# Performance work log

Measured on AMD Instinct MI355X. Metric: run time of the kernel, lower is better.

## Reference

```python
import jax, jax.numpy as jnp
import numpy as np

B, L, HID, NH = 8, 512, 768, 12
D = HID // NH
T_HOP, T_EDGE = 32, 64


def setup_inputs() -> dict:
    key = jax.random.key(0)
    ks = jax.random.split(key, 18)
    f = lambda k, s, sc=1.0: jax.random.normal(k, s, dtype=jnp.float32) * sc
    return {
        "x": f(ks[0], (B, L, HID)),
        "query_hop_emb": f(ks[1], (T_HOP, HID), 0.05),
        "query_edge_emb": f(ks[2], (T_EDGE, HID), 0.05),
        "key_hop_emb": f(ks[3], (T_HOP, HID), 0.05),
        "key_edge_emb": f(ks[4], (T_EDGE, HID), 0.05),
        "value_hop_emb": f(ks[5], (T_HOP, HID), 0.05),
        "value_edge_emb": f(ks[6], (T_EDGE, HID), 0.05),
        "hop": jax.random.randint(ks[7], (B, L, L), 0, T_HOP, dtype=jnp.int32),
        "edge_matrix": jax.random.randint(ks[8], (B, L, L), 0, T_EDGE, dtype=jnp.int32),
        "Wq": f(ks[9], (HID, HID), 0.02), "bq": f(ks[10], (HID,), 0.02),
        "Wk": f(ks[11], (HID, HID), 0.02), "bk": f(ks[12], (HID,), 0.02),
        "Wv": f(ks[13], (HID, HID), 0.02), "bv": f(ks[14], (HID,), 0.02),
        "Wo": f(ks[15], (HID, HID), 0.02), "bo": f(ks[16], (HID,), 0.02),
    }


def reference(x, query_hop_emb, query_edge_emb, key_hop_emb, key_edge_emb,
              value_hop_emb, value_edge_emb, hop, edge_matrix,
              Wq, bq, Wk, bk, Wv, bv, Wo, bo):
    b, l, _ = x.shape
    scale = 1.0 / np.sqrt(D).astype(np.float32)
    heads = lambda t: t.reshape(b, l, NH, D).transpose(0, 2, 1, 3)  # [B,H,L,D]
    emb = lambda t: t.reshape(-1, NH, D)                             # [T,H,D]

    q = heads(x @ Wq + bq)
    k = heads(x @ Wk + bk)
    v = heads(x @ Wv + bv)

    hop_idx = jnp.broadcast_to(hop[:, None], (b, NH, l, l))
    edge_idx = jnp.broadcast_to(edge_matrix[:, None], (b, NH, l, l))

    def bias(t, e, idx):
        # project onto type embeddings then gather per (i,j) type: [B,H,L,L]
        proj = jnp.einsum('bhld,thd->bhlt', t, emb(e))
        return jnp.take_along_axis(proj, idx, axis=3)

    scores = jnp.einsum('bhld,bhmd->bhlm', q, k)
    scores = scores + bias(q, query_hop_emb, hop_idx) + bias(q, query_edge_emb, edge_idx)
    scores = scores + bias(k, key_hop_emb, hop_idx) + bias(k, key_edge_emb, edge_idx)
    att = jax.nn.softmax(scores * scale, axis=3)

    def scatter_by_type(a, idx, T):
        # re-aggregate attention weights per hop/edge type: [B,H,L,T]
        bi = jnp.arange(b)[:, None, None, None]
        hi = jnp.arange(NH)[None, :, None, None]
        li = jnp.arange(l)[None, None, :, None]
        return jnp.zeros((b, NH, l, T), a.dtype).at[bi, hi, li, idx].add(a)

    out = jnp.einsum('bhlm,bhmd->bhld', att, v)
    out = out + jnp.einsum('bhlt,thd->bhld', scatter_by_type(att, hop_idx, T_HOP), emb(value_hop_emb))
    out = out + jnp.einsum('bhlt,thd->bhld', scatter_by_type(att, edge_idx, T_EDGE), emb(value_edge_emb))

    out = out.transpose(0, 2, 1, 3).reshape(b, l, NH * D)
    return out @ Wo + bo
```

## Files before the change

kernel.cpp:

```cpp
#include <hip/hip_runtime.h>
#include <stdint.h>

#define B_   8
#define L_   512
#define HID_ 768
#define NH_  12
#define D_   64
#define BH_  96
#define TT_  96

typedef __attribute__((ext_vector_type(8))) short short8;
typedef __attribute__((ext_vector_type(4))) float fv4;

#define MFMA16(a, b, c) __builtin_amdgcn_mfma_f32_16x16x32_bf16((a), (b), (c), 0, 0, 0)

__device__ __forceinline__ float bf2f(uint16_t h) {
  union { uint32_t u; float f; } c; c.u = ((uint32_t)h) << 16; return c.f;
}
__device__ __forceinline__ uint16_t f2bf(float x) {
  union { float f; uint32_t u; } c; c.f = x;
  uint32_t r = (c.u + 0x7FFFu + ((c.u >> 16) & 1u)) >> 16;
  return (uint16_t)r;
}
__device__ __forceinline__ float clampf(float v, float lim) {
  return fminf(fmaxf(v, -lim), lim);
}

__device__ __forceinline__ void gld_lds16(const uint16_t* g, uint16_t* lds) {
  __builtin_amdgcn_global_load_lds(
      (const __attribute__((address_space(1))) uint32_t*)(uintptr_t)g,
      (__attribute__((address_space(3))) uint32_t*)(uintptr_t)lds, 16, 0, 0);
}

__device__ __forceinline__ int detect_fp32(const void* xraw) {
  const uint16_t* r = (const uint16_t*)xraw;
  int cnt = 0;
#pragma unroll
  for (int j = 0; j < 16; j++) {
    uint16_t u = r[2 * j];
    int e = (u >> 7) & 0xFF;
    if (u != 0 && e >= 100 && e <= 140) cnt++;
  }
  return cnt < 10;
}

#define SEG_X    0
#define SEG_QH   3145728
#define SEG_QE   3170304
#define SEG_KH   3219456
#define SEG_KE   3244032
#define SEG_VH   3293184
#define SEG_VE   3317760
#define SEG_BQ   3366912
#define SEG_BK   3367680
#define SEG_BV   3368448
#define SEG_BO   3369216
#define SEG_END  3369984
#define SEG_VET  3369984
#define SEG_PK   3443712
#define SEG_ALL  5540864

__global__ __launch_bounds__(256) void convert_all(
    const void* __restrict__ x, const void* __restrict__ qh,
    const void* __restrict__ qe, const void* __restrict__ kh,
    const void* __restrict__ ke, const void* __restrict__ vh,
    const void* __restrict__ ve, const void* __restrict__ b0,
    const void* __restrict__ b1, const void* __restrict__ b2,
    const void* __restrict__ b3, const int* __restrict__ hop,
    const int* __restrict__ edge, uint16_t* __restrict__ dst,
    uint16_t* __restrict__ VET, uint16_t* __restrict__ PKs) {
  const int gid = blockIdx.x * 256 + threadIdx.x;
  if (gid >= SEG_ALL) return;
  const int f = detect_fp32(x);
  if (gid >= SEG_PK) {
    const int g = gid - SEG_PK;
    const int j = g & 511;
    const int i = (g >> 9) & 511;
    const int b = g >> 18;
    const int it = i >> 6, w = (i >> 4) & 3, quad = (i >> 2) & 3, r = i & 3;
    const int jc = j >> 6, ni = (j >> 4) & 3, l16 = j & 15;
    const int lane = quad * 16 + l16;
    const size_t didx =
        ((((size_t)(b * 8 + it) * 4 + w) * 8 + jc) * 64 + lane) * 16 + r * 4 +
        ni;
    PKs[didx] = (uint16_t)((hop[g] & 31) | ((edge[g] & 63) << 8));
    return;
  }
  if (gid >= SEG_VET) {
    const int g = gid - SEG_VET;
    const int t = g % TT_;
    const int d = (g / TT_) % D_;
    const int hh = g / (TT_ * D_);
    const void* src = (t < 32) ? vh : ve;
    const size_t idx = (size_t)(t < 32 ? t : t - 32) * HID_ + hh * D_ + d;
    VET[g] = f ? f2bf(((const float*)src)[idx]) : ((const uint16_t*)src)[idx];
    return;
  }
  const void* src;
  int local;
  if (gid < SEG_QH)      { src = x;  local = gid - SEG_X; }
  else if (gid < SEG_QE) { src = qh; local = gid - SEG_QH; }
  else if (gid < SEG_KH) { src = qe; local = gid - SEG_QE; }
  else if (gid < SEG_KE) { src = kh; local = gid - SEG_KH; }
  else if (gid < SEG_VH) { src = ke; local = gid - SEG_KE; }
  else if (gid < SEG_VE) { src = vh; local = gid - SEG_VH; }
  else if (gid < SEG_BQ) { src = ve; local = gid - SEG_VE; }
  else if (gid < SEG_BK) { src = b0; local = gid - SEG_BQ; }
  else if (gid < SEG_BV) { src = b1; local = gid - SEG_BK; }
  else if (gid < SEG_BO) { src = b2; local = gid - SEG_BV; }
  else                   { src = b3; local = gid - SEG_BO; }
  if (f)
    dst[gid] = f2bf(((const float*)src)[local]);
  else
    dst[gid] = ((const uint16_t*)src)[local];
}

__global__ __launch_bounds__(256) void tr_any4(
    const void* __restrict__ s0, const void* __restrict__ s1,
    const void* __restrict__ s2, const void* __restrict__ s3,
    uint16_t* __restrict__ dstbase) {
  __shared__ uint16_t t[32][33];
  const int z = blockIdx.z;
  const void* src = (z == 0) ? s0 : (z == 1) ? s1 : (z == 2) ? s2 : s3;
  uint16_t* dst = dstbase + (size_t)z * (768 * 768);
  const int fp32 = detect_fp32(s0);
  const int tx = threadIdx.x, ty = threadIdx.y;
  const int r0 = blockIdx.y * 32, c0 = blockIdx.x * 32;
#pragma unroll
  for (int k = 0; k < 4; k++) {
    size_t idx = (size_t)(r0 + ty + k * 8) * 768 + c0 + tx;
    t[ty + k * 8][tx] =
        fp32 ? f2bf(((const float*)src)[idx]) : ((const uint16_t*)src)[idx];
  }
  __syncthreads();
#pragma unroll
  for (int k = 0; k < 4; k++)
    dst[(size_t)(c0 + ty + k * 8) * 768 + r0 + tx] = t[tx][ty + k * 8];
}

__global__ __launch_bounds__(256) void gemm128(
    const uint16_t* __restrict__ A,
    const uint16_t* __restrict__ BT0, const uint16_t* __restrict__ BT1,
    const uint16_t* __restrict__ BT2,
    const uint16_t* __restrict__ bias0, const uint16_t* __restrict__ bias1,
    const uint16_t* __restrict__ bias2,
    uint16_t* __restrict__ out, uint16_t* __restrict__ vt) {
  const int z = blockIdx.z;
  const uint16_t* BT = (z == 0) ? BT0 : (z == 1) ? BT1 : BT2;
  const uint16_t* bias = (z == 0) ? bias0 : (z == 1) ? bias1 : bias2;

  __shared__ __align__(16) uint16_t As[128 * 32];
  __shared__ __align__(16) uint16_t Bs[128 * 32];

  const int tid = threadIdx.x;
  const int lane = tid & 63, quad = lane >> 4, l16 = lane & 15;
  const int w = tid >> 6, wm = w & 1, wn = w >> 1;
  const int m0 = blockIdx.x * 128, n0 = blockIdx.y * 128;

  fv4 acc[4][4];
#pragma unroll
  for (int i = 0; i < 4; i++)
#pragma unroll
    for (int j = 0; j < 4; j++) acc[i][j] = (fv4){0.f, 0.f, 0.f, 0.f};

  const int c0 = tid, c1 = tid + 256;
  const int r0 = c0 >> 2, g0 = (c0 & 3) ^ ((r0 >> 1) & 3);
  const int r1 = c1 >> 2, g1 = (c1 & 3) ^ ((r1 >> 1) & 3);
  const uint16_t* A0 = A + (size_t)(m0 + r0) * HID_ + g0 * 8;
  const uint16_t* A1 = A + (size_t)(m0 + r1) * HID_ + g1 * 8;
  const uint16_t* B0 = BT + (size_t)(n0 + r0) * HID_ + g0 * 8;
  const uint16_t* B1 = BT + (size_t)(n0 + r1) * HID_ + g1 * 8;
  uint16_t* lA0 = &As[c0 * 8];
  uint16_t* lA1 = &As[c1 * 8];
  uint16_t* lB0 = &Bs[c0 * 8];
  uint16_t* lB1 = &Bs[c1 * 8];

  int aoff[4], boff[4];
#pragma unroll
  for (int mi = 0; mi < 4; mi++) {
    int row = wm * 64 + mi * 16 + l16;
    aoff[mi] = row * 32 + (quad ^ ((row >> 1) & 3)) * 8;
  }
#pragma unroll
  for (int ni = 0; ni < 4; ni++) {
    int row = wn * 64 + ni * 16 + l16;
    boff[ni] = row * 32 + (quad ^ ((row >> 1) & 3)) * 8;
  }

  for (int k0 = 0; k0 < HID_; k0 += 32) {
    __syncthreads();
    gld_lds16(A0 + k0, lA0);
    gld_lds16(A1 + k0, lA1);
    gld_lds16(B0 + k0, lB0);
    gld_lds16(B1 + k0, lB1);
    __syncthreads();
    short8 af[4], bf[4];
#pragma unroll
    for (int mi = 0; mi < 4; mi++) af[mi] = *(const short8*)&As[aoff[mi]];
#pragma unroll
    for (int ni = 0; ni < 4; ni++) bf[ni] = *(const short8*)&Bs[boff[ni]];
#pragma unroll
    for (int mi = 0; mi < 4; mi++)
#pragma unroll
      for (int ni = 0; ni < 4; ni++)
        acc[mi][ni] = MFMA16(af[mi], bf[ni], acc[mi][ni]);
  }

#pragma unroll
  for (int mi = 0; mi < 4; mi++) {
#pragma unroll
    for (int ni = 0; ni < 4; ni++) {
      const int gn = n0 + wn * 64 + ni * 16 + l16;
      const float bv = bf2f(bias[gn]);
      const int gm0 = m0 + wm * 64 + mi * 16 + quad * 4;
      if (z == 2) {
        const int bb = gm0 >> 9, ll0 = gm0 & 511;
        const int hh = gn >> 6, dd = gn & 63;
        ushort4 pk;
        pk.x = f2bf(clampf(acc[mi][ni][0] + bv, 1e4f));
        pk.y = f2bf(clampf(acc[mi][ni][1] + bv, 1e4f));
        pk.z = f2bf(clampf(acc[mi][ni][2] + bv, 1e4f));
        pk.w = f2bf(clampf(acc[mi][ni][3] + bv, 1e4f));
        *(ushort4*)&vt[(((size_t)(bb * NH_ + hh)) * D_ + dd) * L_ + ll0] = pk;
      } else {
#pragma unroll
        for (int r = 0; r < 4; r++) {
          const int gm = gm0 + r;
          const float fval = clampf(acc[mi][ni][r] + bv, 1e4f);
          uint16_t* O = out + (size_t)z * ((size_t)BH_ * L_ * D_);
          const int bb = gm >> 9, ll = gm & 511, hh = gn >> 6, dd = gn & 63;
          O[(((size_t)(bb * NH_ + hh)) * L_ + ll) * D_ + dd] = f2bf(fval);
        }
      }
    }
  }
}

__global__ __launch_bounds__(256) void gemm64o(
    const uint16_t* __restrict__ A, const uint16_t* __restrict__ BT,
    const uint16_t* __restrict__ bias, float* __restrict__ out) {
  __shared__ __align__(16) uint16_t As[64 * 32];
  __shared__ __align__(16) uint16_t Bs[64 * 32];

  const int tid = threadIdx.x;
  const int lane = tid & 63, quad = lane >> 4, l16 = lane & 15;
  const int w = tid >> 6, wm = w & 1, wn = w >> 1;
  const int m0 = blockIdx.x * 64, n0 = blockIdx.y * 64;

  fv4 acc[2][2];
#pragma unroll
  for (int i = 0; i < 2; i++)
#pragma unroll
    for (int j = 0; j < 2; j++) acc[i][j] = (fv4){0.f, 0.f, 0.f, 0.f};

  const int c0 = tid;
  const int r0 = c0 >> 2, g0 = (c0 & 3) ^ ((r0 >> 1) & 3);
  const uint16_t* A0 = A + (size_t)(m0 + r0) * HID_ + g0 * 8;
  const uint16_t* B0 = BT + (size_t)(n0 + r0) * HID_ + g0 * 8;
  uint16_t* lA0 = &As[c0 * 8];
  uint16_t* lB0 = &Bs[c0 * 8];

  int aoff[2], boff[2];
#pragma unroll
  for (int mi = 0; mi < 2; mi++) {
    int row = wm * 32 + mi * 16 + l16;
    aoff[mi] = row * 32 + (quad ^ ((row >> 1) & 3)) * 8;
  }
#pragma unroll
  for (int ni = 0; ni < 2; ni++) {
    int row = wn * 32 + ni * 16 + l16;
    boff[ni] = row * 32 + (quad ^ ((row >> 1) & 3)) * 8;
  }

  for (int k0 = 0; k0 < HID_; k0 += 32) {
    __syncthreads();
    gld_lds16(A0 + k0, lA0);
    gld_lds16(B0 + k0, lB0);
    __syncthreads();
    short8 af[2], bf[2];
#pragma unroll
    for (int mi = 0; mi < 2; mi++) af[mi] = *(const short8*)&As[aoff[mi]];
#pragma unroll
    for (int ni = 0; ni < 2; ni++) bf[ni] = *(const short8*)&Bs[boff[ni]];
#pragma unroll
    for (int mi = 0; mi < 2; mi++)
#pragma unroll
      for (int ni = 0; ni < 2; ni++)
        acc[mi][ni] = MFMA16(af[mi], bf[ni], acc[mi][ni]);
  }

#pragma unroll
  for (int mi = 0; mi < 2; mi++) {
#pragma unroll
    for (int ni = 0; ni < 2; ni++) {
      const int gn = n0 + wn * 32 + ni * 16 + l16;
      const float bv = bf2f(bias[gn]);
#pragma unroll
      for (int r = 0; r < 4; r++) {
        const int gm = m0 + wm * 32 + mi * 16 + quad * 4 + r;
        out[(size_t)gm * HID_ + gn] = clampf(acc[mi][ni][r] + bv, 1e4f);
      }
    }
  }
}

#define SCALE_FX 4194304.f
#define INV_SCALE_FX 2.38418579e-7f
#define UBC 40.f

__global__ __launch_bounds__(256, 3) void attn_kernel(
    const uint16_t* __restrict__ Q, const uint16_t* __restrict__ Km,
    const uint16_t* __restrict__ Vt,
    const uint16_t* __restrict__ qh, const uint16_t* __restrict__ qe,
    const uint16_t* __restrict__ kh, const uint16_t* __restrict__ ke,
    const uint16_t* __restrict__ VET, const uint16_t* __restrict__ PKs,
    uint16_t* __restrict__ AO) {
  const int n = blockIdx.x;
  const int h = n % NH_;
  const int t2 = n / NH_;
  const int it = t2 & 7, b = t2 >> 3;
  const int bh = b * NH_ + h;
  const int tid = threadIdx.x;
  const int w = tid >> 6, lane = tid & 63, quad = lane >> 4, l16 = lane & 15;
  const int gi = it * 64 + w * 16;

  __shared__ uint16_t cbs[4][16][98];
  __shared__ unsigned bkt[4][16][97];
  __shared__ __align__(16) uint16_t Pw[4][16][72];

  for (int k = lane; k < 16 * 97; k += 64)
    (&bkt[0][0][0])[w * 16 * 97 + k] = 0u;

  const size_t qkb = (size_t)bh * (L_ * D_);
  short8 a0 = *(const short8*)&Q[qkb + (size_t)(gi + l16) * D_ + quad * 8];
  short8 a1 = *(const short8*)&Q[qkb + (size_t)(gi + l16) * D_ + 32 + quad * 8];
  short8 kq0 = *(const short8*)&Km[qkb + (size_t)(gi + l16) * D_ + quad * 8];
  short8 kq1 =
      *(const short8*)&Km[qkb + (size_t)(gi + l16) * D_ + 32 + quad * 8];

  float hx[4] = {-1e30f, -1e30f, -1e30f, -1e30f};
  float ex[4] = {-1e30f, -1e30f, -1e30f, -1e30f};
#pragma unroll
  for (int nt = 0; nt < 6; nt++) {
    const uint16_t* eq;
    const uint16_t* ek;
    int t;
    if (nt < 2) { eq = qh; ek = kh; t = nt * 16 + l16; }
    else        { eq = qe; ek = ke; t = (nt - 2) * 16 + l16; }
    const size_t eb0 = (size_t)t * HID_ + h * D_;
    short8 bq0 = *(const short8*)&eq[eb0 + quad * 8];
    short8 bq1 = *(const short8*)&eq[eb0 + 32 + quad * 8];
    short8 bk0 = *(const short8*)&ek[eb0 + quad * 8];
    short8 bk1 = *(const short8*)&ek[eb0 + 32 + quad * 8];
    fv4 cc = (fv4){0.f, 0.f, 0.f, 0.f};
    cc = MFMA16(a0, bq0, cc);
    cc = MFMA16(a1, bq1, cc);
    cc = MFMA16(kq0, bk0, cc);
    cc = MFMA16(kq1, bk1, cc);
#pragma unroll
    for (int r = 0; r < 4; r++) {
      const float cv = clampf(cc[r], 1e4f);
      cbs[w][quad * 4 + r][nt * 16 + l16] = f2bf(cv);
      if (nt < 2) hx[r] = fmaxf(hx[r], cv);
      else        ex[r] = fmaxf(ex[r], cv);
    }
  }

  float mx[4];
#pragma unroll
  for (int r = 0; r < 4; r++) {
    float mh = hx[r], me = ex[r];
    mh = fmaxf(mh, __shfl_xor(mh, 1, 16));
    mh = fmaxf(mh, __shfl_xor(mh, 2, 16));
    mh = fmaxf(mh, __shfl_xor(mh, 4, 16));
    mh = fmaxf(mh, __shfl_xor(mh, 8, 16));
    me = fmaxf(me, __shfl_xor(me, 1, 16));
    me = fmaxf(me, __shfl_xor(me, 2, 16));
    me = fmaxf(me, __shfl_xor(me, 4, 16));
    me = fmaxf(me, __shfl_xor(me, 8, 16));
    mx[r] = mh + me + UBC;
  }

  const uint16_t* pkw =
      PKs + (((size_t)(b * 8 + it) * 4 + w) * 8) * (64 * 16);
  const size_t vtb = (size_t)bh * (D_ * L_);

  fv4 oacc[4];
#pragma unroll
  for (int ni = 0; ni < 4; ni++) oacc[ni] = (fv4){0.f, 0.f, 0.f, 0.f};
  float lsr[4] = {0.f, 0.f, 0.f, 0.f};

  for (int jc = 0; jc < 8; jc++) {
    short8 pk0 = *(const short8*)&pkw[jc * 1024 + lane * 16];
    short8 pk1 = *(const short8*)&pkw[jc * 1024 + lane * 16 + 8];

    fv4 sacc[4];
#pragma unroll
    for (int ni = 0; ni < 4; ni++) {
      const int key = jc * 64 + ni * 16 + l16;
      short8 kb0 = *(const short8*)&Km[qkb + (size_t)key * D_ + quad * 8];
      short8 kb1 = *(const short8*)&Km[qkb + (size_t)key * D_ + 32 + quad * 8];
      fv4 a = (fv4){0.f, 0.f, 0.f, 0.f};
      a = MFMA16(a0, kb0, a);
      sacc[ni] = MFMA16(a1, kb1, a);
    }

    int thv[16], tev[16];
#pragma unroll
    for (int k = 0; k < 16; k++) {
      const uint32_t pk = (uint16_t)((k < 8) ? pk0[k] : pk1[k - 8]);
      thv[k] = pk & 31;
      tev[k] = (pk >> 8) & 63;
    }
    float bsum[16];
#pragma unroll
    for (int k = 0; k < 16; k++) {
      const int row = quad * 4 + (k >> 2);
      bsum[k] = bf2f(cbs[w][row][thv[k]]) + bf2f(cbs[w][row][32 + tev[k]]);
    }
    float pv[16];
#pragma unroll
    for (int k = 0; k < 16; k++) {
      const int r = k >> 2;
      const float s = sacc[k & 3][r] + bsum[k];
      const float p = __expf((s - mx[r]) * 0.125f);
      pv[k] = p;
      lsr[r] += p;
    }
#pragma unroll
    for (int k = 0; k < 16; k++) {
      const int row = quad * 4 + (k >> 2);
      const unsigned pfx = (unsigned)(pv[k] * SCALE_FX + 0.5f);
      atomicAdd(&bkt[w][row][thv[k]], pfx);
      atomicAdd(&bkt[w][row][32 + tev[k]], pfx);
      Pw[w][row][(k & 3) * 16 + l16] = f2bf(pv[k]);
    }

#pragma unroll
    for (int kc = 0; kc < 2; kc++) {
      short8 pa = *(const short8*)&Pw[w][l16][kc * 32 + quad * 8];
#pragma unroll
      for (int ni = 0; ni < 4; ni++) {
        short8 vb = *(const short8*)&Vt[vtb + (size_t)(ni * 16 + l16) * L_ +
                                        jc * 64 + kc * 32 + quad * 8];
        oacc[ni] = MFMA16(pa, vb, oacc[ni]);
      }
    }
  }

  const uint16_t* vet = VET + (size_t)h * D_ * TT_;
#pragma unroll
  for (int kc = 0; kc < 3; kc++) {
    short8 pa;
#pragma unroll
    for (int j = 0; j < 8; j++)
      pa[j] = (short)f2bf((float)bkt[w][l16][kc * 32 + quad * 8 + j] *
                          INV_SCALE_FX);
#pragma unroll
    for (int ni = 0; ni < 4; ni++) {
      short8 vb =
          *(const short8*)&vet[(size_t)(ni * 16 + l16) * TT_ + kc * 32 +
                               quad * 8];
      oacc[ni] = MFMA16(pa, vb, oacc[ni]);
    }
  }

  float linv[4];
#pragma unroll
  for (int r = 0; r < 4; r++) {
    float s = lsr[r];
    s += __shfl_xor(s, 1, 16);
    s += __shfl_xor(s, 2, 16);
    s += __shfl_xor(s, 4, 16);
    s += __shfl_xor(s, 8, 16);
    linv[r] = 1.f / s;
  }

#pragma unroll
  for (int ni = 0; ni < 4; ni++)
#pragma unroll
    for (int r = 0; r < 4; r++) {
      const int i = gi + quad * 4 + r;
      AO[(((size_t)b * L_ + i) * NH_ + h) * D_ + ni * 16 + l16] =
          f2bf(oacc[ni][r] * linv[r]);
    }
}

extern "C" void kernel_launch(void* const* d_in, const int* in_sizes, int n_in,
                              void* d_out, int out_size, void* d_ws,
                              size_t ws_size, hipStream_t stream) {
  const void* x_raw = d_in[0];
  const int* hop    = (const int*)d_in[7];
  const int* edge   = (const int*)d_in[8];

  char* ws = (char*)d_ws;
  uint16_t* QKV = (uint16_t*)(ws);
  uint16_t* Qp  = QKV;
  uint16_t* Kp  = QKV + (size_t)BH_ * L_ * D_;
  uint16_t* Vtp = (uint16_t*)(ws + 18874368);
  uint16_t* PKs = (uint16_t*)(ws + 25165824);
  uint16_t* AO  = (uint16_t*)(ws + 44040192);
  uint16_t* WTq = (uint16_t*)(ws + 50331648);
  uint16_t* WTk = WTq + 768 * 768;
  uint16_t* WTv = WTk + 768 * 768;
  uint16_t* WTo = WTv + 768 * 768;
  uint16_t* CAN = (uint16_t*)(ws + 55050240);
  uint16_t* VET = (uint16_t*)(ws + 61790208);

  uint16_t* xc  = CAN + SEG_X;
  uint16_t* qhc = CAN + SEG_QH;
  uint16_t* qec = CAN + SEG_QE;
  uint16_t* khc = CAN + SEG_KH;
  uint16_t* kec = CAN + SEG_KE;
  uint16_t* bqc = CAN + SEG_BQ;
  uint16_t* bkc = CAN + SEG_BK;
  uint16_t* bvc = CAN + SEG_BV;
  uint16_t* boc = CAN + SEG_BO;

  convert_all<<<(SEG_ALL + 255) / 256, 256, 0, stream>>>(
      x_raw, d_in[1], d_in[2], d_in[3], d_in[4], d_in[5], d_in[6],
      d_in[10], d_in[12], d_in[14], d_in[16], hop, edge, CAN, VET, PKs);

  dim3 tb(32, 8, 1);
  tr_any4<<<dim3(24, 24, 4), tb, 0, stream>>>(d_in[9], d_in[11], d_in[13],
                                              d_in[15], WTq);

  gemm128<<<dim3(32, 6, 3), 256, 0, stream>>>(xc, WTq, WTk, WTv, bqc, bkc,
                                              bvc, QKV, Vtp);

  attn_kernel<<<768, 256, 0, stream>>>(Qp, Kp, Vtp, qhc, qec, khc, kec, VET,
                                       PKs, AO);

  gemm64o<<<dim3(64, 12), 256, 0, stream>>>(AO, WTo, boc, (float*)d_out);
}
```

Baseline: 225.6 us.

## Deepen output GEMM K-tile and prefetch next K/type chunk in attention loop

The output projection GEMM now stages 64-wide K tiles instead of 32, halving the number of barrier-separated load phases and using an 8-way XOR swizzle for the wider LDS rows. In the attention kernel, the K-matrix fragments and packed hop/edge type words for the next key chunk are loaded into registers before the current chunk is computed, so global load latency overlaps with the MFMA and softmax work. This costs more registers, which may lower occupancy, and the last iteration issues a redundant wrapped-around prefetch.

```diff
diff --git a/kernel.cpp b/kernel.cpp
--- a/kernel.cpp
+++ b/kernel.cpp
@@ -239,8 +239,8 @@
 __global__ __launch_bounds__(256) void gemm64o(
     const uint16_t* __restrict__ A, const uint16_t* __restrict__ BT,
     const uint16_t* __restrict__ bias, float* __restrict__ out) {
-  __shared__ __align__(16) uint16_t As[64 * 32];
-  __shared__ __align__(16) uint16_t Bs[64 * 32];
+  __shared__ __align__(16) uint16_t As[64 * 64];
+  __shared__ __align__(16) uint16_t Bs[64 * 64];
 
   const int tid = threadIdx.x;
   const int lane = tid & 63, quad = lane >> 4, l16 = lane & 15;
@@ -253,40 +253,54 @@
 #pragma unroll
     for (int j = 0; j < 2; j++) acc[i][j] = (fv4){0.f, 0.f, 0.f, 0.f};
 
-  const int c0 = tid;
-  const int r0 = c0 >> 2, g0 = (c0 & 3) ^ ((r0 >> 1) & 3);
+  const int c0 = tid, c1 = tid + 256;
+  const int r0 = c0 >> 3, g0 = (c0 & 7) ^ (r0 & 7);
+  const int r1 = c1 >> 3, g1 = (c1 & 7) ^ (r1 & 7);
   const uint16_t* A0 = A + (size_t)(m0 + r0) * HID_ + g0 * 8;
+  const uint16_t* A1 = A + (size_t)(m0 + r1) * HID_ + g1 * 8;
   const uint16_t* B0 = BT + (size_t)(n0 + r0) * HID_ + g0 * 8;
+  const uint16_t* B1 = BT + (size_t)(n0 + r1) * HID_ + g1 * 8;
   uint16_t* lA0 = &As[c0 * 8];
+  uint16_t* lA1 = &As[c1 * 8];
   uint16_t* lB0 = &Bs[c0 * 8];
-
-  int aoff[2], boff[2];
+  uint16_t* lB1 = &Bs[c1 * 8];
+
+  int aoff[2][2], boff[2][2];
 #pragma unroll
   for (int mi = 0; mi < 2; mi++) {
-    int row = wm * 32 + mi * 16 + l16;
-    aoff[mi] = row * 32 + (quad ^ ((row >> 1) & 3)) * 8;
+    const int row = wm * 32 + mi * 16 + l16;
+#pragma unroll
+    for (int kc = 0; kc < 2; kc++)
+      aoff[mi][kc] = row * 64 + ((kc * 4 + quad) ^ (row & 7)) * 8;
   }
 #pragma unroll
   for (int ni = 0; ni < 2; ni++) {
-    int row = wn * 32 + ni * 16 + l16;
-    boff[ni] = row * 32 + (quad ^ ((row >> 1) & 3)) * 8;
-  }
-
-  for (int k0 = 0; k0 < HID_; k0 += 32) {
+    const int row = wn * 32 + ni * 16 + l16;
+#pragma unroll
+    for (int kc = 0; kc < 2; kc++)
+      boff[ni][kc] = row * 64 + ((kc * 4 + quad) ^ (row & 7)) * 8;
+  }
+
+  for (int k0 = 0; k0 < HID_; k0 += 64) {
     __syncthreads();
     gld_lds16(A0 + k0, lA0);
+    gld_lds16(A1 + k0, lA1);
     gld_lds16(B0 + k0, lB0);
+    gld_lds16(B1 + k0, lB1);
     __syncthreads();
-    short8 af[2], bf[2];
-#pragma unroll
-    for (int mi = 0; mi < 2; mi++) af[mi] = *(const short8*)&As[aoff[mi]];
-#pragma unroll
-    for (int ni = 0; ni < 2; ni++) bf[ni] = *(const short8*)&Bs[boff[ni]];
-#pragma unroll
-    for (int mi = 0; mi < 2; mi++)
-#pragma unroll
-      for (int ni = 0; ni < 2; ni++)
-        acc[mi][ni] = MFMA16(af[mi], bf[ni], acc[mi][ni]);
+#pragma unroll
+    for (int kc = 0; kc < 2; kc++) {
+      short8 af[2], bf[2];
+#pragma unroll
+      for (int mi = 0; mi < 2; mi++) af[mi] = *(const short8*)&As[aoff[mi][kc]];
+#pragma unroll
+      for (int ni = 0; ni < 2; ni++) bf[ni] = *(const short8*)&Bs[boff[ni][kc]];
+#pragma unroll
+      for (int mi = 0; mi < 2; mi++)
+#pragma unroll
+        for (int ni = 0; ni < 2; ni++)
+          acc[mi][ni] = MFMA16(af[mi], bf[ni], acc[mi][ni]);
+    }
   }
 
 #pragma unroll
@@ -390,25 +404,40 @@
   for (int ni = 0; ni < 4; ni++) oacc[ni] = (fv4){0.f, 0.f, 0.f, 0.f};
   float lsr[4] = {0.f, 0.f, 0.f, 0.f};
 
+  short8 ckb0[4], ckb1[4];
+#pragma unroll
+  for (int ni = 0; ni < 4; ni++) {
+    const int key = ni * 16 + l16;
+    ckb0[ni] = *(const short8*)&Km[qkb + (size_t)key * D_ + quad * 8];
+    ckb1[ni] = *(const short8*)&Km[qkb + (size_t)key * D_ + 32 + quad * 8];
+  }
+  short8 cpk0 = *(const short8*)&pkw[lane * 16];
+  short8 cpk1 = *(const short8*)&pkw[lane * 16 + 8];
+
   for (int jc = 0; jc < 8; jc++) {
-    short8 pk0 = *(const short8*)&pkw[jc * 1024 + lane * 16];
-    short8 pk1 = *(const short8*)&pkw[jc * 1024 + lane * 16 + 8];
+    const int jn = (jc + 1) & 7;
+    short8 nkb0[4], nkb1[4];
+#pragma unroll
+    for (int ni = 0; ni < 4; ni++) {
+      const int key = jn * 64 + ni * 16 + l16;
+      nkb0[ni] = *(const short8*)&Km[qkb + (size_t)key * D_ + quad * 8];
+      nkb1[ni] = *(const short8*)&Km[qkb + (size_t)key * D_ + 32 + quad * 8];
+    }
+    short8 npk0 = *(const short8*)&pkw[jn * 1024 + lane * 16];
+    short8 npk1 = *(const short8*)&pkw[jn * 1024 + lane * 16 + 8];
 
     fv4 sacc[4];
 #pragma unroll
     for (int ni = 0; ni < 4; ni++) {
-      const int key = jc * 64 + ni * 16 + l16;
-      short8 kb0 = *(const short8*)&Km[qkb + (size_t)key * D_ + quad * 8];
-      short8 kb1 = *(const short8*)&Km[qkb + (size_t)key * D_ + 32 + quad * 8];
       fv4 a = (fv4){0.f, 0.f, 0.f, 0.f};
-      a = MFMA16(a0, kb0, a);
-      sacc[ni] = MFMA16(a1, kb1, a);
+      a = MFMA16(a0, ckb0[ni], a);
+      sacc[ni] = MFMA16(a1, ckb1[ni], a);
     }
 
     int thv[16], tev[16];
 #pragma unroll
     for (int k = 0; k < 16; k++) {
-      const uint32_t pk = (uint16_t)((k < 8) ? pk0[k] : pk1[k - 8]);
+      const uint32_t pk = (uint16_t)((k < 8) ? cpk0[k] : cpk1[k - 8]);
       thv[k] = pk & 31;
       tev[k] = (pk >> 8) & 63;
     }
@@ -446,6 +475,14 @@
         oacc[ni] = MFMA16(pa, vb, oacc[ni]);
       }
     }
+
+#pragma unroll
+    for (int ni = 0; ni < 4; ni++) {
+      ckb0[ni] = nkb0[ni];
+      ckb1[ni] = nkb1[ni];
+    }
+    cpk0 = npk0;
+    cpk1 = npk1;
   }
 
   const uint16_t* vet = VET + (size_t)h * D_ * TT_;
```

Result: no change. 225.2 us (-0.1%).
